# Optimization experiments

Measured on AMD Instinct MI355X. Metric: run time of the kernel, lower is better.

## Reference

```python
import jax, jax.numpy as jnp
import numpy as np
from jax import lax

N, M, T, V, C_IN, C_OUT, KT, PAD = 16, 2, 300, 25, 64, 64, 9, 4
BN_EPS = 1e-5

# NTU-RGB+D 25-joint skeleton edges (0-indexed), symmetric, plus self-loops
_NTU_EDGES = [(0,1),(1,20),(2,20),(3,2),(4,20),(5,4),(6,5),(7,6),(8,20),(9,8),
              (10,9),(11,10),(12,0),(13,12),(14,13),(15,14),(16,0),(17,16),
              (18,17),(19,18),(21,22),(22,7),(23,24),(24,11)]

def _build_adj():
    A = np.zeros((V, V), dtype=np.float32)
    for i, j in _NTU_EDGES:
        A[i, j] = 1.0
        A[j, i] = 1.0
    A += np.eye(V, dtype=np.float32)  # self-loops (DGL GCN preprocessing)
    return jnp.asarray(A)


def setup_inputs() -> dict:
    key = jax.random.key(0)
    ks = jax.random.split(key, 8)
    stdv = 1.0 / np.sqrt(C_OUT)
    # conv_init: normal(0, sqrt(2/(out_channels*prod(kernel))))
    conv_std = np.sqrt(2.0 / (C_OUT * KT * 1))
    return {
        "h": jax.random.normal(ks[0], (N * M * T * V, C_IN), dtype=jnp.float32),
        "adj": _build_adj(),
        "gcn_w": jax.random.uniform(ks[1], (C_IN, C_OUT), minval=-stdv, maxval=stdv, dtype=jnp.float32),
        "gcn_b": jax.random.uniform(ks[2], (C_OUT,), minval=-stdv, maxval=stdv, dtype=jnp.float32),
        "conv_w": conv_std * jax.random.normal(ks[3], (C_OUT, C_OUT, KT, 1), dtype=jnp.float32),
        "conv_b": jnp.zeros((C_OUT,), dtype=jnp.float32),
        "bn_gamma": jnp.ones((C_OUT,), dtype=jnp.float32),
        "bn_beta": jnp.zeros((C_OUT,), dtype=jnp.float32),
        "bn_mean": 0.1 * jax.random.normal(ks[4], (C_OUT,), dtype=jnp.float32),
        "bn_var": jax.random.uniform(ks[5], (C_OUT,), minval=0.5, maxval=1.5, dtype=jnp.float32),
    }


def reference(h, adj, gcn_w, gcn_b, conv_w, conv_b, bn_gamma, bn_beta, bn_mean, bn_var):
    # ---- GCNLayer (dropout is identity at eval) ----
    # symmetric norm = deg^{-1/2}, identical across the N*M*T copies of the skeleton
    norm = adj.sum(axis=1) ** -0.5                      # (V,)
    x = h @ gcn_w                                        # (N*M*T*V, C_OUT)
    x = x.reshape(-1, V, C_OUT) * norm[:, None]          # pre-norm scale
    x = jnp.einsum('vu,buc->bvc', adj, x)                # copy_src + sum aggregation
    x = x * norm[:, None] + gcn_b                        # post-norm scale + bias
    x = jax.nn.relu(x)

    # ---- TemporalConvNetwork ----
    v = x.reshape(N, M, T, V, C_OUT)
    v = v.transpose(0, 1, 4, 2, 3).reshape(N * M, C_OUT, T, V)   # (NM, C, T, V)
    v = lax.conv_general_dilated(v, conv_w, window_strides=(1, 1),
                                 padding=[(PAD, PAD), (0, 0)],
                                 dimension_numbers=('NCHW', 'OIHW', 'NCHW'))
    v = v + conv_b[None, :, None, None]
    inv_std = bn_gamma / jnp.sqrt(bn_var + BN_EPS)       # eval-mode BatchNorm2d
    v = (v - bn_mean[None, :, None, None]) * inv_std[None, :, None, None] + bn_beta[None, :, None, None]
    v = jax.nn.relu(v)
    v = v.reshape(N, M, C_OUT, T, V).transpose(0, 1, 3, 4, 2)    # (N, M, T, V, C)

    # ---- residual (downt is None since in_feats == out_feats and stride == 1) ----
    return v + h.reshape(N, M, T, V, C_IN)
```

## Files before the change

kernel.cpp:

```cpp
#include <hip/hip_runtime.h>
#include <hip/hip_bf16.h>


typedef __bf16 bf16x8 __attribute__((ext_vector_type(8)));
typedef __bf16 bf16x4 __attribute__((ext_vector_type(4)));
typedef float  f32x4  __attribute__((ext_vector_type(4)));

#define Y_OFF   0
#define WC2_OFF 30720000
#define WGT_OFF 30793728
#define A2P_OFF 30801920
#define SC_OFF  30803968
#define SH_OFF  30804224

__global__ __launch_bounds__(256) void prep_kernel(
    const float* __restrict__ adj, const float* __restrict__ gcn_w,
    const float* __restrict__ conv_w, const float* __restrict__ conv_b,
    const float* __restrict__ bn_g, const float* __restrict__ bn_b,
    const float* __restrict__ bn_m, const float* __restrict__ bn_v,
    __bf16* __restrict__ wc2, __bf16* __restrict__ wgt,
    __bf16* __restrict__ a2p, float* __restrict__ scale, float* __restrict__ shift) {
  int tid = threadIdx.x;
  for (int e = blockIdx.x * 256 + tid; e < 36864; e += gridDim.x * 256) {
    int j = e & 7, t1 = e >> 3, c = t1 & 63, g = t1 >> 6;
    int kap = g * 8 + j, kt = kap >> 6, ci = kap & 63;
    wc2[e] = (__bf16)conv_w[(c * 64 + ci) * 9 + kt];
  }
  if (blockIdx.x == 0) {
    for (int e = tid; e < 4096; e += 256) {
      int c = e >> 6, k = e & 63;
      wgt[e] = (__bf16)gcn_w[k * 64 + c];
    }
  } else if (blockIdx.x == 1) {
    for (int e = tid; e < 1024; e += 256) {
      int v = e >> 5, u = e & 31;
      float val = 0.f;
      if (v < 25 && u < 25) {
        float dv = 0.f, du = 0.f;
        for (int t = 0; t < 25; ++t) { dv += adj[v * 25 + t]; du += adj[u * 25 + t]; }
        val = rsqrtf(dv) * adj[v * 25 + u] * rsqrtf(du);
      }
      a2p[e] = (__bf16)val;
    }
  } else if (blockIdx.x == 2) {
    if (tid < 64) {
      float sc = bn_g[tid] * rsqrtf(bn_v[tid] + 1e-5f);
      scale[tid] = sc;
      shift[tid] = (conv_b[tid] - bn_m[tid]) * sc + bn_b[tid];
    }
  }
}

__global__ __launch_bounds__(256) void gcn_kernel(
    const float* __restrict__ h, const __bf16* __restrict__ wgt_g,
    const __bf16* __restrict__ a2p_g, const float* __restrict__ gcn_b,
    __bf16* __restrict__ y) {
  __shared__ __align__(16) __bf16 wgT[4096];
  __shared__ __align__(16) __bf16 a2p[1024];
  __shared__ __align__(16) __bf16 hb[4][32 * 72];
  __shared__ __align__(16) __bf16 x1t[4][64 * 40];
  int tid = threadIdx.x, w = tid >> 6, lane = tid & 63;
  int l15 = lane & 15, quad = lane >> 4;

  {
    const uint4* src = (const uint4*)wgt_g; uint4* dst = (uint4*)wgT;
    for (int e = tid; e < 512; e += 256) dst[e] = src[e];
    const uint4* s2 = (const uint4*)a2p_g; uint4* d2 = (uint4*)a2p;
    if (tid < 128) d2[tid] = s2[tid];
  }
  __syncthreads();

  int skel = blockIdx.x * 4 + w;
  for (int e = lane; e < 7 * 72; e += 64) hb[w][25 * 72 + e] = (__bf16)0.f;
  for (int it = 0; it < 7; ++it) {
    int u = it * 4 + quad;
    if (u < 25) {
      float4 hv = *(const float4*)&h[(skel * 25 + u) * 64 + l15 * 4];
      bf16x4 b; b[0] = (__bf16)hv.x; b[1] = (__bf16)hv.y; b[2] = (__bf16)hv.z; b[3] = (__bf16)hv.w;
      *(bf16x4*)&hb[w][u * 72 + l15 * 4] = b;
    }
  }
  for (int mt = 0; mt < 4; ++mt)
    for (int nt = 0; nt < 2; ++nt) {
      f32x4 acc = {0.f, 0.f, 0.f, 0.f};
      for (int kk = 0; kk < 2; ++kk) {
        bf16x8 a = *(const bf16x8*)&wgT[(mt * 16 + l15) * 64 + kk * 32 + quad * 8];
        bf16x8 b = *(const bf16x8*)&hb[w][(nt * 16 + l15) * 72 + kk * 32 + quad * 8];
        acc = __builtin_amdgcn_mfma_f32_16x16x32_bf16(a, b, acc, 0, 0, 0);
      }
      int u = nt * 16 + l15, c0 = mt * 16 + quad * 4;
      for (int r = 0; r < 4; ++r) x1t[w][(c0 + r) * 40 + u] = (__bf16)acc[r];
    }
  for (int mt = 0; mt < 4; ++mt)
    for (int nt = 0; nt < 2; ++nt) {
      f32x4 acc = {0.f, 0.f, 0.f, 0.f};
      bf16x8 a = *(const bf16x8*)&x1t[w][(mt * 16 + l15) * 40 + quad * 8];
      bf16x8 b = *(const bf16x8*)&a2p[(nt * 16 + l15) * 32 + quad * 8];
      acc = __builtin_amdgcn_mfma_f32_16x16x32_bf16(a, b, acc, 0, 0, 0);
      int v = nt * 16 + l15, c0 = mt * 16 + quad * 4;
      if (v < 25) {
        float4 bias = *(const float4*)&gcn_b[c0];
        bf16x4 o;
        o[0] = (__bf16)fmaxf(acc[0] + bias.x, 0.f);
        o[1] = (__bf16)fmaxf(acc[1] + bias.y, 0.f);
        o[2] = (__bf16)fmaxf(acc[2] + bias.z, 0.f);
        o[3] = (__bf16)fmaxf(acc[3] + bias.w, 0.f);
        *(bf16x4*)&y[skel * 1600 + v * 64 + c0] = o;
      }
    }
}

__global__ __launch_bounds__(256) void conv_kernel(
    const __bf16* __restrict__ y, const __bf16* __restrict__ wc2,
    const float* __restrict__ scale, const float* __restrict__ shift,
    const float* __restrict__ h, float* __restrict__ out) {
  __shared__ __align__(16) __bf16 ylds[264 * 72];
  int tid = threadIdx.x, w = tid >> 6, lane = tid & 63;
  int l15 = lane & 15, quad = lane >> 4;
  int tb = blockIdx.x, vv = blockIdx.y, nm = blockIdx.z;
  int t0 = tb * 256;
  {
    int seg = tid & 7;
    for (int row = tid >> 3; row < 264; row += 32) {
      int tg = t0 - 4 + row;
      uint4 val = {0u, 0u, 0u, 0u};
      if (tg >= 0 && tg < 300)
        val = *(const uint4*)&y[((nm * 300 + tg) * 25 + vv) * 64 + seg * 8];
      *(uint4*)&ylds[row * 72 + seg * 8] = val;
    }
  }
  __syncthreads();
  int wt0 = t0 + w * 64;
  if (wt0 >= 300) return;
  f32x4 acc[4][4];
  for (int m = 0; m < 4; ++m) for (int n = 0; n < 4; ++n) acc[m][n] = (f32x4){0.f, 0.f, 0.f, 0.f};
  for (int kk = 0; kk < 18; ++kk) {
    bf16x8 a[4];
    const __bf16* wbase = wc2 + ((kk * 4 + quad) * 64) * 8;
    for (int m = 0; m < 4; ++m) a[m] = *(const bf16x8*)&wbase[(m * 16 + l15) * 8];
    int kt = kk >> 1, cib = (kk & 1) * 32 + quad * 8;
    for (int n = 0; n < 4; ++n) {
      bf16x8 b = *(const bf16x8*)&ylds[(w * 64 + n * 16 + l15 + kt) * 72 + cib];
      for (int m = 0; m < 4; ++m)
        acc[m][n] = __builtin_amdgcn_mfma_f32_16x16x32_bf16(a[m], b, acc[m][n], 0, 0, 0);
    }
  }
  for (int n = 0; n < 4; ++n) {
    int tt = wt0 + n * 16 + l15;
    if (tt >= 300) continue;
    for (int m = 0; m < 4; ++m) {
      int c0 = m * 16 + quad * 4;
      int idx = ((nm * 300 + tt) * 25 + vv) * 64 + c0;
      float4 sc = *(const float4*)&scale[c0];
      float4 sh = *(const float4*)&shift[c0];
      float4 hr = *(const float4*)&h[idx];
      float4 o;
      o.x = fmaxf(acc[m][n][0] * sc.x + sh.x, 0.f) + hr.x;
      o.y = fmaxf(acc[m][n][1] * sc.y + sh.y, 0.f) + hr.y;
      o.z = fmaxf(acc[m][n][2] * sc.z + sh.z, 0.f) + hr.z;
      o.w = fmaxf(acc[m][n][3] * sc.w + sh.w, 0.f) + hr.w;
      *(float4*)&out[idx] = o;
    }
  }
}

extern "C" void kernel_launch(void* const* d_in, const int* in_sizes, int n_in,
                              void* d_out, int out_size, void* d_ws, size_t ws_size,
                              hipStream_t stream) {
  const float* h      = (const float*)d_in[0];
  const float* adj    = (const float*)d_in[1];
  const float* gcn_w  = (const float*)d_in[2];
  const float* gcn_b  = (const float*)d_in[3];
  const float* conv_w = (const float*)d_in[4];
  const float* conv_b = (const float*)d_in[5];
  const float* bn_g   = (const float*)d_in[6];
  const float* bn_b   = (const float*)d_in[7];
  const float* bn_m   = (const float*)d_in[8];
  const float* bn_v   = (const float*)d_in[9];
  float* out = (float*)d_out;
  char* ws = (char*)d_ws;

  __bf16* y_ws   = (__bf16*)(ws + Y_OFF);
  __bf16* wc2    = (__bf16*)(ws + WC2_OFF);
  __bf16* wgt    = (__bf16*)(ws + WGT_OFF);
  __bf16* a2p    = (__bf16*)(ws + A2P_OFF);
  float*  scale  = (float*)(ws + SC_OFF);
  float*  shift  = (float*)(ws + SH_OFF);

  prep_kernel<<<64, 256, 0, stream>>>(adj, gcn_w, conv_w, conv_b, bn_g, bn_b, bn_m, bn_v,
                                      wc2, wgt, a2p, scale, shift);
  gcn_kernel<<<2400, 256, 0, stream>>>(h, wgt, a2p, gcn_b, y_ws);
  conv_kernel<<<dim3(2, 25, 32), 256, 0, stream>>>(y_ws, wc2, scale, shift, h, out);
}
```

Measured before the change: 195.1 us.

## Transpose GCN output layout and remap conv to per-wave time tiles

The GCN kernel stages its result in LDS and writes y in an (nm, v, t, c) layout, so each conv wave reads a contiguous time window for one joint. The conv kernel is remapped so each wave independently handles a 64-step time tile, with the last tile overlapping. This removes the block-wide barrier and the wasted waves that fell past T. It also adds an XOR-swizzled LDS layout, double-buffered weight-register loads, and padded LDS strides in the GCN kernel to reduce bank conflicts. In exchange, GCN stores become strided across joints, and some time steps are computed and written twice.

Result: faster. 172.6 us (-11.5%).

```diff
diff --git a/kernel.cpp b/kernel.cpp
--- a/kernel.cpp
+++ b/kernel.cpp
@@ -55,22 +55,27 @@
     const float* __restrict__ h, const __bf16* __restrict__ wgt_g,
     const __bf16* __restrict__ a2p_g, const float* __restrict__ gcn_b,
     __bf16* __restrict__ y) {
-  __shared__ __align__(16) __bf16 wgT[4096];
-  __shared__ __align__(16) __bf16 a2p[1024];
+  __shared__ __align__(16) __bf16 wgT[64 * 72];
+  __shared__ __align__(16) __bf16 a2p[32 * 40];
   __shared__ __align__(16) __bf16 hb[4][32 * 72];
   __shared__ __align__(16) __bf16 x1t[4][64 * 40];
   int tid = threadIdx.x, w = tid >> 6, lane = tid & 63;
   int l15 = lane & 15, quad = lane >> 4;
 
   {
-    const uint4* src = (const uint4*)wgt_g; uint4* dst = (uint4*)wgT;
-    for (int e = tid; e < 512; e += 256) dst[e] = src[e];
-    const uint4* s2 = (const uint4*)a2p_g; uint4* d2 = (uint4*)a2p;
-    if (tid < 128) d2[tid] = s2[tid];
+    for (int e = tid; e < 512; e += 256) {
+      uint4 val = ((const uint4*)wgt_g)[e];
+      *(uint4*)&wgT[(e >> 3) * 72 + (e & 7) * 8] = val;
+    }
+    if (tid < 128) {
+      uint4 val = ((const uint4*)a2p_g)[tid];
+      *(uint4*)&a2p[(tid >> 2) * 40 + (tid & 3) * 8] = val;
+    }
   }
   __syncthreads();
 
   int skel = blockIdx.x * 4 + w;
+  int nm = skel / 300, tloc = skel - nm * 300;
   for (int e = lane; e < 7 * 72; e += 64) hb[w][25 * 72 + e] = (__bf16)0.f;
   for (int it = 0; it < 7; ++it) {
     int u = it * 4 + quad;
@@ -84,7 +89,7 @@
     for (int nt = 0; nt < 2; ++nt) {
       f32x4 acc = {0.f, 0.f, 0.f, 0.f};
       for (int kk = 0; kk < 2; ++kk) {
-        bf16x8 a = *(const bf16x8*)&wgT[(mt * 16 + l15) * 64 + kk * 32 + quad * 8];
+        bf16x8 a = *(const bf16x8*)&wgT[(mt * 16 + l15) * 72 + kk * 32 + quad * 8];
         bf16x8 b = *(const bf16x8*)&hb[w][(nt * 16 + l15) * 72 + kk * 32 + quad * 8];
         acc = __builtin_amdgcn_mfma_f32_16x16x32_bf16(a, b, acc, 0, 0, 0);
       }
@@ -95,59 +100,78 @@
     for (int nt = 0; nt < 2; ++nt) {
       f32x4 acc = {0.f, 0.f, 0.f, 0.f};
       bf16x8 a = *(const bf16x8*)&x1t[w][(mt * 16 + l15) * 40 + quad * 8];
-      bf16x8 b = *(const bf16x8*)&a2p[(nt * 16 + l15) * 32 + quad * 8];
+      bf16x8 b = *(const bf16x8*)&a2p[(nt * 16 + l15) * 40 + quad * 8];
       acc = __builtin_amdgcn_mfma_f32_16x16x32_bf16(a, b, acc, 0, 0, 0);
       int v = nt * 16 + l15, c0 = mt * 16 + quad * 4;
       if (v < 25) {
         float4 bias = *(const float4*)&gcn_b[c0];
-        bf16x4 o;
-        o[0] = (__bf16)fmaxf(acc[0] + bias.x, 0.f);
-        o[1] = (__bf16)fmaxf(acc[1] + bias.y, 0.f);
-        o[2] = (__bf16)fmaxf(acc[2] + bias.z, 0.f);
-        o[3] = (__bf16)fmaxf(acc[3] + bias.w, 0.f);
-        *(bf16x4*)&y[skel * 1600 + v * 64 + c0] = o;
+        hb[w][v * 80 + c0 + 0] = (__bf16)fmaxf(acc[0] + bias.x, 0.f);
+        hb[w][v * 80 + c0 + 1] = (__bf16)fmaxf(acc[1] + bias.y, 0.f);
+        hb[w][v * 80 + c0 + 2] = (__bf16)fmaxf(acc[2] + bias.z, 0.f);
+        hb[w][v * 80 + c0 + 3] = (__bf16)fmaxf(acc[3] + bias.w, 0.f);
       }
     }
+  for (int e = lane; e < 200; e += 64) {
+    int v = e >> 3, ch = e & 7;
+    uint4 val = *(const uint4*)&hb[w][v * 80 + ch * 8];
+    *(uint4*)&y[((nm * 25 + v) * 300 + tloc) * 64 + ch * 8] = val;
+  }
 }
 
 __global__ __launch_bounds__(256) void conv_kernel(
     const __bf16* __restrict__ y, const __bf16* __restrict__ wc2,
     const float* __restrict__ scale, const float* __restrict__ shift,
     const float* __restrict__ h, float* __restrict__ out) {
-  __shared__ __align__(16) __bf16 ylds[264 * 72];
+  __shared__ __align__(16) __bf16 ylds[4 * 72 * 64];
   int tid = threadIdx.x, w = tid >> 6, lane = tid & 63;
   int l15 = lane & 15, quad = lane >> 4;
-  int tb = blockIdx.x, vv = blockIdx.y, nm = blockIdx.z;
-  int t0 = tb * 256;
+  int gid = blockIdx.x * 4 + w;
+  int ti = gid % 5, r1 = gid / 5;
+  int vv = r1 % 25, nm = r1 / 25;
+  int t0 = (ti < 4) ? ti * 64 : 236;
+
+  __bf16* my = &ylds[w * 4608];
   {
-    int seg = tid & 7;
-    for (int row = tid >> 3; row < 264; row += 32) {
-      int tg = t0 - 4 + row;
+    const __bf16* ybase = &y[((nm * 25 + vv) * 300) * 64];
+    uint4 stg[9];
+    for (int it = 0; it < 9; ++it) {
+      int idx = it * 64 + lane, r = idx >> 3, ch = idx & 7;
+      int tg = t0 - 4 + r;
       uint4 val = {0u, 0u, 0u, 0u};
-      if (tg >= 0 && tg < 300)
-        val = *(const uint4*)&y[((nm * 300 + tg) * 25 + vv) * 64 + seg * 8];
-      *(uint4*)&ylds[row * 72 + seg * 8] = val;
-    }
-  }
-  __syncthreads();
-  int wt0 = t0 + w * 64;
-  if (wt0 >= 300) return;
+      if (tg >= 0 && tg < 300) val = *(const uint4*)&ybase[tg * 64 + ch * 8];
+      stg[it] = val;
+    }
+    for (int it = 0; it < 9; ++it) {
+      int idx = it * 64 + lane, r = idx >> 3, ch = idx & 7;
+      *(uint4*)&my[r * 64 + ((ch ^ (r & 7)) * 8)] = stg[it];
+    }
+  }
+
   f32x4 acc[4][4];
   for (int m = 0; m < 4; ++m) for (int n = 0; n < 4; ++n) acc[m][n] = (f32x4){0.f, 0.f, 0.f, 0.f};
-  for (int kk = 0; kk < 18; ++kk) {
-    bf16x8 a[4];
-    const __bf16* wbase = wc2 + ((kk * 4 + quad) * 64) * 8;
-    for (int m = 0; m < 4; ++m) a[m] = *(const bf16x8*)&wbase[(m * 16 + l15) * 8];
-    int kt = kk >> 1, cib = (kk & 1) * 32 + quad * 8;
-    for (int n = 0; n < 4; ++n) {
-      bf16x8 b = *(const bf16x8*)&ylds[(w * 64 + n * 16 + l15 + kt) * 72 + cib];
-      for (int m = 0; m < 4; ++m)
-        acc[m][n] = __builtin_amdgcn_mfma_f32_16x16x32_bf16(a[m], b, acc[m][n], 0, 0, 0);
-    }
-  }
+
+  bf16x8 a0[4], a1[4];
+#define LOADA(dst, kk_) { const __bf16* wb = wc2 + (((kk_) * 4 + quad) * 64) * 8; \
+    for (int m = 0; m < 4; ++m) dst[m] = *(const bf16x8*)&wb[(m * 16 + l15) * 8]; }
+#define COMPUTE(kk_, areg) { int kt = (kk_) >> 1, chb = ((kk_) & 1) * 4 + quad; \
+    for (int n = 0; n < 4; ++n) { \
+      int row = n * 16 + l15 + kt; \
+      bf16x8 b = *(const bf16x8*)&my[row * 64 + ((chb ^ (row & 7)) * 8)]; \
+      for (int m = 0; m < 4; ++m) \
+        acc[m][n] = __builtin_amdgcn_mfma_f32_16x16x32_bf16(areg[m], b, acc[m][n], 0, 0, 0); \
+    } }
+  LOADA(a0, 0)
+  for (int kk = 0; kk < 18; kk += 2) {
+    LOADA(a1, kk + 1)
+    COMPUTE(kk, a0)
+    if (kk + 2 < 18) LOADA(a0, kk + 2)
+    COMPUTE(kk + 1, a1)
+  }
+#undef LOADA
+#undef COMPUTE
+
   for (int n = 0; n < 4; ++n) {
-    int tt = wt0 + n * 16 + l15;
-    if (tt >= 300) continue;
+    int tt = t0 + n * 16 + l15;
     for (int m = 0; m < 4; ++m) {
       int c0 = m * 16 + quad * 4;
       int idx = ((nm * 300 + tt) * 25 + vv) * 64 + c0;
@@ -190,5 +214,5 @@
   prep_kernel<<<64, 256, 0, stream>>>(adj, gcn_w, conv_w, conv_b, bn_g, bn_b, bn_m, bn_v,
                                       wc2, wgt, a2p, scale, shift);
   gcn_kernel<<<2400, 256, 0, stream>>>(h, wgt, a2p, gcn_b, y_ws);
-  conv_kernel<<<dim3(2, 25, 32), 256, 0, stream>>>(y_ws, wc2, scale, shift, h, out);
-}
+  conv_kernel<<<1000, 256, 0, stream>>>(y_ws, wc2, scale, shift, h, out);
+}
```
